# Optimization experiments

Hardware: AMD Instinct MI355X
Metric: run time of the kernel (lower is better)

## Reference

```python
import jax, jax.numpy as jnp
import numpy as np

DIM = 1024
NHEAD = 16
HEAD_DIM = DIM // NHEAD
MAX_REL = 256
B, S = 4, 2048


def setup_inputs() -> dict:
    key = jax.random.key(0)
    ks = jax.random.split(key, 10)
    sc = 1.0 / np.sqrt(DIM)
    inp = {
        "x": jax.random.normal(ks[0], (B, S, DIM), jnp.float32),
        "Wq": jax.random.normal(ks[1], (DIM, DIM), jnp.float32) * sc,
        "bq": jnp.zeros((DIM,), jnp.float32),
        "Wk": jax.random.normal(ks[2], (DIM, DIM), jnp.float32) * sc,
        "bk": jnp.zeros((DIM,), jnp.float32),
        "Wv": jax.random.normal(ks[3], (DIM, DIM), jnp.float32) * sc,
        "bv": jnp.zeros((DIM,), jnp.float32),
        "Wo": jax.random.normal(ks[4], (DIM, DIM), jnp.float32) * sc,
        "bo": jnp.zeros((DIM,), jnp.float32),
        "rel_bias": jax.random.normal(ks[5], (2 * MAX_REL + 1, NHEAD), jnp.float32) * 0.02,
    }
    return inp


def reference(x, Wq, bq, Wk, bk, Wv, bv, Wo, bo, rel_bias):
    b, s, d = x.shape
    h, hd = NHEAD, HEAD_DIM
    # projections (torch Linear: x @ W.T + b)
    q = (x @ Wq.T + bq).reshape(b, s, h, hd).transpose(0, 2, 1, 3)
    k = (x @ Wk.T + bk).reshape(b, s, h, hd).transpose(0, 2, 1, 3)
    v = (x @ Wv.T + bv).reshape(b, s, h, hd).transpose(0, 2, 1, 3)
    scale = hd ** (-0.5)
    scores = jnp.einsum('bhqd,bhkd->bhqk', q, k) * scale
    # relative position bias: gather [S,S,H] -> [H,S,S]
    rel = jnp.clip(jnp.arange(s)[:, None] - jnp.arange(s)[None, :], -MAX_REL, MAX_REL) + MAX_REL
    bias = rel_bias[rel].transpose(2, 0, 1)  # [H,S,S]
    scores = scores + bias[None]
    probs = jax.nn.softmax(scores, axis=-1)
    out = jnp.einsum('bhqk,bhkd->bhqd', probs, v)
    out = out.transpose(0, 2, 1, 3).reshape(b, s, d)
    return out @ Wo.T + bo
```

## Files before the change

### kernel.cpp

```cpp
#include <hip/hip_runtime.h>
#include <hip/hip_bf16.h>
#include <stdint.h>

#define DIM    1024
#define NHEAD  16
#define HD     64
#define MAXREL 256
#define BB     4
#define SS     2048
#define MM     (BB*SS)

typedef float f32x4 __attribute__((ext_vector_type(4)));
typedef short s16x8 __attribute__((ext_vector_type(8)));

__device__ __forceinline__ ushort f2bf(float f) {
  union { float f; uint32_t u; } v; v.f = f;
  uint32_t r = v.u + 0x7FFFu + ((v.u >> 16) & 1u);
  return (ushort)(r >> 16);
}

__device__ __forceinline__ ushort f2bf_hw(float f) {
  __hip_bfloat16 h = __float2bfloat16(f);
  return *reinterpret_cast<ushort*>(&h);
}

__global__ void cast_kernel(const float* __restrict__ in, ushort* __restrict__ out, int n4) {
  int i = blockIdx.x * blockDim.x + threadIdx.x;
  if (i < n4) {
    float4 v = reinterpret_cast<const float4*>(in)[i];
    ushort4 o; o.x = f2bf(v.x); o.y = f2bf(v.y); o.z = f2bf(v.z); o.w = f2bf(v.w);
    reinterpret_cast<ushort4*>(out)[i] = o;
  }
}

__global__ void cast4_kernel(const float* __restrict__ w0, const float* __restrict__ w1,
                             const float* __restrict__ w2, const float* __restrict__ w3,
                             ushort* __restrict__ out) {
  int i = blockIdx.x * blockDim.x + threadIdx.x;
  int which = i >> 18;
  int j = i & ((1 << 18) - 1);
  const float* src = (which == 0) ? w0 : (which == 1) ? w1 : (which == 2) ? w2 : w3;
  float4 v = reinterpret_cast<const float4*>(src)[j];
  ushort4 o; o.x = f2bf(v.x); o.y = f2bf(v.y); o.z = f2bf(v.z); o.w = f2bf(v.w);
  reinterpret_cast<ushort4*>(out)[i] = o;
}

__global__ __launch_bounds__(256) void gemm_qkv(
    const ushort* __restrict__ A, const ushort* __restrict__ W,
    const float* __restrict__ bq, const float* __restrict__ bk, const float* __restrict__ bv,
    ushort* __restrict__ Qo, ushort* __restrict__ Ko, ushort* __restrict__ Vto) {
  __shared__ ushort At[128 * 64];
  __shared__ ushort Bt[128 * 64];
  const int tid = threadIdx.x;
  const int lane = tid & 63, w = tid >> 6;
  const int g = lane >> 4, c16 = lane & 15;
  const int ln8 = lane >> 3, l8 = lane & 7;
  const int bid = blockIdx.x;
  const int xcd = bid & 7, j = bid >> 3;
  const int by = xcd * 8 + (j & 7), bx = j >> 3;
  const int m0 = by * 128, n0 = bx * 128;
  const int wm = w >> 1, wn = w & 1;
  const int slotp = l8 ^ ln8;

  f32x4 acc[4][4];
#pragma unroll
  for (int i = 0; i < 4; i++)
#pragma unroll
    for (int jj = 0; jj < 4; jj++) acc[i][jj] = f32x4{0.f, 0.f, 0.f, 0.f};

  for (int k0 = 0; k0 < DIM; k0 += 64) {
    __syncthreads();
#pragma unroll
    for (int t = 0; t < 4; t++) {
      int seg = w * 4 + t;
      const ushort* ga = A + (size_t)(m0 + seg * 8 + ln8) * DIM + k0 + slotp * 8;
      __builtin_amdgcn_global_load_lds((const __attribute__((address_space(1))) void*)ga,
          (__attribute__((address_space(3))) void*)(At + seg * 512), 16, 0, 0);
      const ushort* gb = W + (size_t)(n0 + seg * 8 + ln8) * DIM + k0 + slotp * 8;
      __builtin_amdgcn_global_load_lds((const __attribute__((address_space(1))) void*)gb,
          (__attribute__((address_space(3))) void*)(Bt + seg * 512), 16, 0, 0);
    }
    __syncthreads();

#pragma unroll
    for (int kk = 0; kk < 2; kk++) {
      s16x8 af[4], bfr[4];
#pragma unroll
      for (int mi = 0; mi < 4; mi++) {
        int row = wm * 64 + mi * 16 + c16;
        int slot = (kk * 4 + g) ^ (row & 7);
        af[mi] = *(const s16x8*)(At + row * 64 + slot * 8);
      }
#pragma unroll
      for (int ni = 0; ni < 4; ni++) {
        int row = wn * 64 + ni * 16 + c16;
        int slot = (kk * 4 + g) ^ (row & 7);
        bfr[ni] = *(const s16x8*)(Bt + row * 64 + slot * 8);
      }
#pragma unroll
      for (int mi = 0; mi < 4; mi++)
#pragma unroll
        for (int ni = 0; ni < 4; ni++)
          acc[mi][ni] = __builtin_amdgcn_mfma_f32_16x16x32_bf16(af[mi], bfr[ni], acc[mi][ni], 0, 0, 0);
    }
  }

  const int which = n0 >> 10;
  const float* bp = (which == 0) ? bq : (which == 1) ? bk : bv;
  ushort* qk = (which == 0) ? Qo : Ko;
#pragma unroll
  for (int mi = 0; mi < 4; mi++)
#pragma unroll
    for (int ni = 0; ni < 4; ni++)
#pragma unroll
      for (int r = 0; r < 4; r++) {
        int m = m0 + wm * 64 + mi * 16 + g * 4 + r;
        int n = n0 + wn * 64 + ni * 16 + c16;
        int col = n & 1023;
        float v = acc[mi][ni][r] + bp[col];
        int b = m >> 11, s = m & 2047;
        int h = col >> 6, d = col & 63;
        ushort bv16 = f2bf(v);
        if (which < 2)
          qk[((size_t)(b * NHEAD + h) * SS + s) * HD + d] = bv16;
        else
          Vto[((size_t)(b * NHEAD + h) * HD + d) * SS + s] = bv16;
      }
}

__global__ __launch_bounds__(256) void gemm_bt(
    const ushort* __restrict__ A, const ushort* __restrict__ W,
    const float* __restrict__ bias, float* __restrict__ out) {
  __shared__ ushort At[128 * 64];
  __shared__ ushort Bt[128 * 64];
  const int tid = threadIdx.x;
  const int lane = tid & 63, w = tid >> 6;
  const int g = lane >> 4, c16 = lane & 15;
  const int ln8 = lane >> 3, l8 = lane & 7;
  const int bid = blockIdx.x;
  const int xcd = bid & 7, j = bid >> 3;
  const int by = xcd * 8 + (j & 7), bx = j >> 3;
  const int m0 = by * 128, n0 = bx * 128;
  const int wm = w >> 1, wn = w & 1;
  const int slotp = l8 ^ ln8;

  f32x4 acc[4][4];
#pragma unroll
  for (int i = 0; i < 4; i++)
#pragma unroll
    for (int jj = 0; jj < 4; jj++) acc[i][jj] = f32x4{0.f, 0.f, 0.f, 0.f};

  for (int k0 = 0; k0 < DIM; k0 += 64) {
    __syncthreads();
#pragma unroll
    for (int t = 0; t < 4; t++) {
      int seg = w * 4 + t;
      const ushort* ga = A + (size_t)(m0 + seg * 8 + ln8) * DIM + k0 + slotp * 8;
      __builtin_amdgcn_global_load_lds((const __attribute__((address_space(1))) void*)ga,
          (__attribute__((address_space(3))) void*)(At + seg * 512), 16, 0, 0);
      const ushort* gb = W + (size_t)(n0 + seg * 8 + ln8) * DIM + k0 + slotp * 8;
      __builtin_amdgcn_global_load_lds((const __attribute__((address_space(1))) void*)gb,
          (__attribute__((address_space(3))) void*)(Bt + seg * 512), 16, 0, 0);
    }
    __syncthreads();

#pragma unroll
    for (int kk = 0; kk < 2; kk++) {
      s16x8 af[4], bfr[4];
#pragma unroll
      for (int mi = 0; mi < 4; mi++) {
        int row = wm * 64 + mi * 16 + c16;
        int slot = (kk * 4 + g) ^ (row & 7);
        af[mi] = *(const s16x8*)(At + row * 64 + slot * 8);
      }
#pragma unroll
      for (int ni = 0; ni < 4; ni++) {
        int row = wn * 64 + ni * 16 + c16;
        int slot = (kk * 4 + g) ^ (row & 7);
        bfr[ni] = *(const s16x8*)(Bt + row * 64 + slot * 8);
      }
#pragma unroll
      for (int mi = 0; mi < 4; mi++)
#pragma unroll
        for (int ni = 0; ni < 4; ni++)
          acc[mi][ni] = __builtin_amdgcn_mfma_f32_16x16x32_bf16(af[mi], bfr[ni], acc[mi][ni], 0, 0, 0);
    }
  }

#pragma unroll
  for (int mi = 0; mi < 4; mi++)
#pragma unroll
    for (int ni = 0; ni < 4; ni++)
#pragma unroll
      for (int r = 0; r < 4; r++) {
        int m = m0 + wm * 64 + mi * 16 + g * 4 + r;
        int n = n0 + wn * 64 + ni * 16 + c16;
        out[(size_t)m * DIM + n] = acc[mi][ni][r] + bias[n];
      }
}

__global__ __launch_bounds__(256) void attn_kernel(
    const ushort* __restrict__ Qb, const ushort* __restrict__ Kb,
    const ushort* __restrict__ Vt, const float* __restrict__ relb,
    ushort* __restrict__ Ob) {
  __shared__ ushort Kt[64 * 64];
  __shared__ ushort Vtile[64 * 64];
  __shared__ ushort Pt[4][16 * 64];
  __shared__ float btab[516];
  const int tid = threadIdx.x;
  const int lane = tid & 63, w = tid >> 6;
  const int g = lane >> 4, c16 = lane & 15;
  const int ln8 = lane >> 3, l8 = lane & 7;

  const int bid = blockIdx.x;
  const int idx = bid >> 3;
  const int bh = (bid & 7) * 8 + (idx & 7);
  const int qb = idx >> 3;
  const int h = bh & 15, b = bh >> 4;
  const int qw = qb * 64 + w * 16;
  const size_t bhoff = (size_t)bh * SS * HD;
  const int slotp = l8 ^ ln8;

  for (int j = tid; j < 513; j += 256) btab[j] = relb[j * NHEAD + h] * 1.44269504f;

  s16x8 aq[2];
  aq[0] = *(const s16x8*)(Qb + bhoff + (size_t)(qw + c16) * HD + g * 8);
  aq[1] = *(const s16x8*)(Qb + bhoff + (size_t)(qw + c16) * HD + 32 + g * 8);

  f32x4 oacc[4];
#pragma unroll
  for (int i = 0; i < 4; i++) oacc[i] = f32x4{0.f, 0.f, 0.f, 0.f};
  float lacc[4] = {0.f, 0.f, 0.f, 0.f};

  ushort* pw = &Pt[w][0];
  const float SC = 0.180336880f;

  for (int kb = 0; kb < 32; kb++) {
    __syncthreads();
#pragma unroll
    for (int t = 0; t < 2; t++) {
      int seg = w * 2 + t;
      const ushort* gk = Kb + bhoff + (size_t)(kb * 64 + seg * 8 + ln8) * HD + slotp * 8;
      __builtin_amdgcn_global_load_lds((const __attribute__((address_space(1))) void*)gk,
          (__attribute__((address_space(3))) void*)(Kt + seg * 512), 16, 0, 0);
      const ushort* gv = Vt + bhoff + (size_t)(seg * 8 + ln8) * SS + kb * 64 + slotp * 8;
      __builtin_amdgcn_global_load_lds((const __attribute__((address_space(1))) void*)gv,
          (__attribute__((address_space(3))) void*)(Vtile + seg * 512), 16, 0, 0);
    }
    __syncthreads();

    f32x4 sc[4];
    __builtin_amdgcn_s_setprio(1);
#pragma unroll
    for (int cj = 0; cj < 4; cj++) {
      f32x4 z = f32x4{0.f, 0.f, 0.f, 0.f};
#pragma unroll
      for (int kk = 0; kk < 2; kk++) {
        int row = cj * 16 + c16;
        int slot = (kk * 4 + g) ^ (row & 7);
        s16x8 bk = *(const s16x8*)(Kt + row * 64 + slot * 8);
        z = __builtin_amdgcn_mfma_f32_16x16x32_bf16(aq[kk], bk, z, 0, 0, 0);
      }
      sc[cj] = z;
    }
    __builtin_amdgcn_s_setprio(0);

#pragma unroll
    for (int cj = 0; cj < 4; cj++) {
      int kmin = kb * 64 + cj * 16;
      if (qw - (kmin + 15) >= MAXREL) {
        float c = btab[512];
#pragma unroll
        for (int r = 0; r < 4; r++) sc[cj][r] = sc[cj][r] * SC + c;
      } else if (kmin - (qw + 15) >= MAXREL) {
        float c = btab[0];
#pragma unroll
        for (int r = 0; r < 4; r++) sc[cj][r] = sc[cj][r] * SC + c;
      } else {
        int relbase = qw + g * 4 - (kmin + c16);
#pragma unroll
        for (int r = 0; r < 4; r++) {
          int rel = relbase + r;
          rel = (rel < -MAXREL) ? -MAXREL : (rel > MAXREL ? MAXREL : rel);
          sc[cj][r] = sc[cj][r] * SC + btab[rel + MAXREL];
        }
      }
#pragma unroll
      for (int r = 0; r < 4; r++) {
        float p = __builtin_amdgcn_exp2f(sc[cj][r]);
        sc[cj][r] = p;
        lacc[r] += p;
      }
    }
#pragma unroll
    for (int cj = 0; cj < 4; cj++)
#pragma unroll
      for (int r = 0; r < 4; r++) {
        int prow = g * 4 + r, pcol = cj * 16 + c16;
        pw[prow * 64 + (pcol ^ ((prow & 7) << 3))] = f2bf_hw(sc[cj][r]);
      }
    __builtin_amdgcn_s_setprio(1);
#pragma unroll
    for (int kk = 0; kk < 2; kk++) {
      s16x8 ap = *(const s16x8*)(pw + c16 * 64 + ((kk * 32 + g * 8) ^ ((c16 & 7) << 3)));
#pragma unroll
      for (int ni = 0; ni < 4; ni++) {
        int row = ni * 16 + c16;
        int slot = (kk * 4 + g) ^ (row & 7);
        s16x8 bv = *(const s16x8*)(Vtile + row * 64 + slot * 8);
        oacc[ni] = __builtin_amdgcn_mfma_f32_16x16x32_bf16(ap, bv, oacc[ni], 0, 0, 0);
      }
    }
    __builtin_amdgcn_s_setprio(0);
  }

#pragma unroll
  for (int r = 0; r < 4; r++) {
    float rs = lacc[r];
    rs += __shfl_xor(rs, 1); rs += __shfl_xor(rs, 2);
    rs += __shfl_xor(rs, 4); rs += __shfl_xor(rs, 8);
    lacc[r] = 1.f / rs;
  }
#pragma unroll
  for (int ni = 0; ni < 4; ni++)
#pragma unroll
    for (int r = 0; r < 4; r++) {
      int q = qw + g * 4 + r;
      int col = h * 64 + ni * 16 + c16;
      Ob[(size_t)(b * SS + q) * DIM + col] = f2bf_hw(oacc[ni][r] * lacc[r]);
    }
}

extern "C" void kernel_launch(void* const* d_in, const int* in_sizes, int n_in,
                              void* d_out, int out_size, void* d_ws, size_t ws_size,
                              hipStream_t stream) {
  const float* x  = (const float*)d_in[0];
  const float* Wq = (const float*)d_in[1];
  const float* bq = (const float*)d_in[2];
  const float* Wk = (const float*)d_in[3];
  const float* bk = (const float*)d_in[4];
  const float* Wv = (const float*)d_in[5];
  const float* bv = (const float*)d_in[6];
  const float* Wo = (const float*)d_in[7];
  const float* bo = (const float*)d_in[8];
  const float* relb = (const float*)d_in[9];

  uint8_t* ws = (uint8_t*)d_ws;
  ushort* x_bf   = (ushort*)(ws + 0);
  ushort* wq_bf  = (ushort*)(ws + (16u << 20));
  ushort* wo_bf  = (ushort*)(ws + (22u << 20));
  ushort* q_bf   = (ushort*)(ws + (24u << 20));
  ushort* k_bf   = (ushort*)(ws + (40u << 20));
  ushort* vt_bf  = (ushort*)(ws + (56u << 20));
  ushort* at_bf  = (ushort*)(ws + (72u << 20));

  const int NX = MM * DIM / 4;
  cast_kernel<<<NX / 256, 256, 0, stream>>>(x, x_bf, NX);
  cast4_kernel<<<(4 << 18) / 256, 256, 0, stream>>>(Wq, Wk, Wv, Wo, wq_bf);

  gemm_qkv<<<dim3(1536), 256, 0, stream>>>(
      x_bf, wq_bf, bq, bk, bv, q_bf, k_bf, vt_bf);

  attn_kernel<<<dim3(2048), 256, 0, stream>>>(q_bf, k_bf, vt_bf, relb, at_bf);

  gemm_bt<<<dim3(512), 256, 0, stream>>>(at_bf, wo_bf, bo, (float*)d_out);
}
```

Before: 332.2 us.

## Process 32 query rows per wave in attention to reuse K/V tiles

Each wave now handles two 16-row query sub-tiles instead of one, so every block covers 128 queries and the grid is halved. Each K/V tile loaded into LDS, and each K/V fragment read from it, now feeds twice as many MFMAs, which cuts global and LDS traffic per unit of work. The cost is roughly double the accumulator and score registers per thread, which may reduce occupancy, and fewer blocks in the grid.

```diff
diff --git a/kernel.cpp b/kernel.cpp
--- a/kernel.cpp
+++ b/kernel.cpp
@@ -205,7 +205,7 @@
     ushort* __restrict__ Ob) {
   __shared__ ushort Kt[64 * 64];
   __shared__ ushort Vtile[64 * 64];
-  __shared__ ushort Pt[4][16 * 64];
+  __shared__ ushort Pt[4][32 * 64];
   __shared__ float btab[516];
   const int tid = threadIdx.x;
   const int lane = tid & 63, w = tid >> 6;
@@ -217,20 +217,25 @@
   const int bh = (bid & 7) * 8 + (idx & 7);
   const int qb = idx >> 3;
   const int h = bh & 15, b = bh >> 4;
-  const int qw = qb * 64 + w * 16;
+  const int qw = qb * 128 + w * 32;
   const size_t bhoff = (size_t)bh * SS * HD;
   const int slotp = l8 ^ ln8;
 
   for (int j = tid; j < 513; j += 256) btab[j] = relb[j * NHEAD + h] * 1.44269504f;
 
-  s16x8 aq[2];
-  aq[0] = *(const s16x8*)(Qb + bhoff + (size_t)(qw + c16) * HD + g * 8);
-  aq[1] = *(const s16x8*)(Qb + bhoff + (size_t)(qw + c16) * HD + 32 + g * 8);
-
-  f32x4 oacc[4];
-#pragma unroll
-  for (int i = 0; i < 4; i++) oacc[i] = f32x4{0.f, 0.f, 0.f, 0.f};
-  float lacc[4] = {0.f, 0.f, 0.f, 0.f};
+  s16x8 aq[2][2];
+#pragma unroll
+  for (int h2 = 0; h2 < 2; h2++) {
+    aq[h2][0] = *(const s16x8*)(Qb + bhoff + (size_t)(qw + h2 * 16 + c16) * HD + g * 8);
+    aq[h2][1] = *(const s16x8*)(Qb + bhoff + (size_t)(qw + h2 * 16 + c16) * HD + 32 + g * 8);
+  }
+
+  f32x4 oacc[2][4];
+#pragma unroll
+  for (int h2 = 0; h2 < 2; h2++)
+#pragma unroll
+    for (int i = 0; i < 4; i++) oacc[h2][i] = f32x4{0.f, 0.f, 0.f, 0.f};
+  float lacc[2][4] = {{0.f, 0.f, 0.f, 0.f}, {0.f, 0.f, 0.f, 0.f}};
 
   ushort* pw = &Pt[w][0];
   const float SC = 0.180336880f;
@@ -249,86 +254,100 @@
     }
     __syncthreads();
 
-    f32x4 sc[4];
+    f32x4 sc[2][4];
     __builtin_amdgcn_s_setprio(1);
 #pragma unroll
     for (int cj = 0; cj < 4; cj++) {
-      f32x4 z = f32x4{0.f, 0.f, 0.f, 0.f};
+      f32x4 z0 = f32x4{0.f, 0.f, 0.f, 0.f};
+      f32x4 z1 = f32x4{0.f, 0.f, 0.f, 0.f};
 #pragma unroll
       for (int kk = 0; kk < 2; kk++) {
         int row = cj * 16 + c16;
         int slot = (kk * 4 + g) ^ (row & 7);
         s16x8 bk = *(const s16x8*)(Kt + row * 64 + slot * 8);
-        z = __builtin_amdgcn_mfma_f32_16x16x32_bf16(aq[kk], bk, z, 0, 0, 0);
-      }
-      sc[cj] = z;
+        z0 = __builtin_amdgcn_mfma_f32_16x16x32_bf16(aq[0][kk], bk, z0, 0, 0, 0);
+        z1 = __builtin_amdgcn_mfma_f32_16x16x32_bf16(aq[1][kk], bk, z1, 0, 0, 0);
+      }
+      sc[0][cj] = z0; sc[1][cj] = z1;
     }
     __builtin_amdgcn_s_setprio(0);
 
 #pragma unroll
-    for (int cj = 0; cj < 4; cj++) {
-      int kmin = kb * 64 + cj * 16;
-      if (qw - (kmin + 15) >= MAXREL) {
-        float c = btab[512];
-#pragma unroll
-        for (int r = 0; r < 4; r++) sc[cj][r] = sc[cj][r] * SC + c;
-      } else if (kmin - (qw + 15) >= MAXREL) {
-        float c = btab[0];
-#pragma unroll
-        for (int r = 0; r < 4; r++) sc[cj][r] = sc[cj][r] * SC + c;
-      } else {
-        int relbase = qw + g * 4 - (kmin + c16);
+    for (int h2 = 0; h2 < 2; h2++) {
+      int qwh = qw + h2 * 16;
+#pragma unroll
+      for (int cj = 0; cj < 4; cj++) {
+        int kmin = kb * 64 + cj * 16;
+        if (qwh - (kmin + 15) >= MAXREL) {
+          float c = btab[512];
+#pragma unroll
+          for (int r = 0; r < 4; r++) sc[h2][cj][r] = sc[h2][cj][r] * SC + c;
+        } else if (kmin - (qwh + 15) >= MAXREL) {
+          float c = btab[0];
+#pragma unroll
+          for (int r = 0; r < 4; r++) sc[h2][cj][r] = sc[h2][cj][r] * SC + c;
+        } else {
+          int relbase = qwh + g * 4 - (kmin + c16);
+#pragma unroll
+          for (int r = 0; r < 4; r++) {
+            int rel = relbase + r;
+            rel = (rel < -MAXREL) ? -MAXREL : (rel > MAXREL ? MAXREL : rel);
+            sc[h2][cj][r] = sc[h2][cj][r] * SC + btab[rel + MAXREL];
+          }
+        }
 #pragma unroll
         for (int r = 0; r < 4; r++) {
-          int rel = relbase + r;
-          rel = (rel < -MAXREL) ? -MAXREL : (rel > MAXREL ? MAXREL : rel);
-          sc[cj][r] = sc[cj][r] * SC + btab[rel + MAXREL];
+          float p = __builtin_amdgcn_exp2f(sc[h2][cj][r]);
+          sc[h2][cj][r] = p;
+          lacc[h2][r] += p;
         }
       }
-#pragma unroll
-      for (int r = 0; r < 4; r++) {
-        float p = __builtin_amdgcn_exp2f(sc[cj][r]);
-        sc[cj][r] = p;
-        lacc[r] += p;
-      }
-    }
-#pragma unroll
-    for (int cj = 0; cj < 4; cj++)
-#pragma unroll
-      for (int r = 0; r < 4; r++) {
-        int prow = g * 4 + r, pcol = cj * 16 + c16;
-        pw[prow * 64 + (pcol ^ ((prow & 7) << 3))] = f2bf_hw(sc[cj][r]);
-      }
+    }
+#pragma unroll
+    for (int h2 = 0; h2 < 2; h2++)
+#pragma unroll
+      for (int cj = 0; cj < 4; cj++)
+#pragma unroll
+        for (int r = 0; r < 4; r++) {
+          int prow = h2 * 16 + g * 4 + r, pcol = cj * 16 + c16;
+          pw[prow * 64 + (pcol ^ ((prow & 7) << 3))] = f2bf_hw(sc[h2][cj][r]);
+        }
     __builtin_amdgcn_s_setprio(1);
 #pragma unroll
     for (int kk = 0; kk < 2; kk++) {
-      s16x8 ap = *(const s16x8*)(pw + c16 * 64 + ((kk * 32 + g * 8) ^ ((c16 & 7) << 3)));
+      s16x8 ap0 = *(const s16x8*)(pw + (c16) * 64 + ((kk * 32 + g * 8) ^ ((c16 & 7) << 3)));
+      s16x8 ap1 = *(const s16x8*)(pw + (16 + c16) * 64 + ((kk * 32 + g * 8) ^ ((c16 & 7) << 3)));
 #pragma unroll
       for (int ni = 0; ni < 4; ni++) {
         int row = ni * 16 + c16;
         int slot = (kk * 4 + g) ^ (row & 7);
         s16x8 bv = *(const s16x8*)(Vtile + row * 64 + slot * 8);
-        oacc[ni] = __builtin_amdgcn_mfma_f32_16x16x32_bf16(ap, bv, oacc[ni], 0, 0, 0);
+        oacc[0][ni] = __builtin_amdgcn_mfma_f32_16x16x32_bf16(ap0, bv, oacc[0][ni], 0, 0, 0);
+        oacc[1][ni] = __builtin_amdgcn_mfma_f32_16x16x32_bf16(ap1, bv, oacc[1][ni], 0, 0, 0);
       }
     }
     __builtin_amdgcn_s_setprio(0);
   }
 
 #pragma unroll
-  for (int r = 0; r < 4; r++) {
-    float rs = lacc[r];
-    rs += __shfl_xor(rs, 1); rs += __shfl_xor(rs, 2);
-    rs += __shfl_xor(rs, 4); rs += __shfl_xor(rs, 8);
-    lacc[r] = 1.f / rs;
-  }
-#pragma unroll
-  for (int ni = 0; ni < 4; ni++)
+  for (int h2 = 0; h2 < 2; h2++)
 #pragma unroll
     for (int r = 0; r < 4; r++) {
-      int q = qw + g * 4 + r;
-      int col = h * 64 + ni * 16 + c16;
-      Ob[(size_t)(b * SS + q) * DIM + col] = f2bf_hw(oacc[ni][r] * lacc[r]);
-    }
+      float rs = lacc[h2][r];
+      rs += __shfl_xor(rs, 1); rs += __shfl_xor(rs, 2);
+      rs += __shfl_xor(rs, 4); rs += __shfl_xor(rs, 8);
+      lacc[h2][r] = 1.f / rs;
+    }
+#pragma unroll
+  for (int h2 = 0; h2 < 2; h2++)
+#pragma unroll
+    for (int ni = 0; ni < 4; ni++)
+#pragma unroll
+      for (int r = 0; r < 4; r++) {
+        int q = qw + h2 * 16 + g * 4 + r;
+        int col = h * 64 + ni * 16 + c16;
+        Ob[(size_t)(b * SS + q) * DIM + col] = f2bf_hw(oacc[h2][ni][r] * lacc[h2][r]);
+      }
 }
 
 extern "C" void kernel_launch(void* const* d_in, const int* in_sizes, int n_in,
@@ -361,7 +380,7 @@
   gemm_qkv<<<dim3(1536), 256, 0, stream>>>(
       x_bf, wq_bf, bq, bk, bv, q_bf, k_bf, vt_bf);
 
-  attn_kernel<<<dim3(2048), 256, 0, stream>>>(q_bf, k_bf, vt_bf, relb, at_bf);
+  attn_kernel<<<dim3(1024), 256, 0, stream>>>(q_bf, k_bf, vt_bf, relb, at_bf);
 
   gemm_bt<<<dim3(512), 256, 0, stream>>>(at_bf, wo_bf, bo, (float*)d_out);
 }
```

After: 342.0 us. 2.9% more time.
